# Kernel tuning notes

Measured on AMD Instinct MI355X. Metric: run time of the kernel, lower is better.

## Reference

```python
import jax, jax.numpy as jnp
import numpy as np

B, N, D_IN, D, H, L, NQ, NC, HID = 4, 25000, 32, 256, 8, 6, 100, 18, 1024


def _ln(x, g, b, eps=1e-5):
    m = jnp.mean(x, -1, keepdims=True)
    v = jnp.mean((x - m) ** 2, -1, keepdims=True)
    return (x - m) / jnp.sqrt(v + eps) * g + b


def _mha(q, kv, wqkv, bqkv, wo, bo, h):
    # q: (B, Lq, d), kv: (B, Lk, d); torch nn.MultiheadAttention math
    d = q.shape[-1]
    dh = d // h
    wq, wk, wv = jnp.split(wqkv, 3, axis=0)
    bq, bk, bv = jnp.split(bqkv, 3)
    Q = (q @ wq.T + bq).reshape(q.shape[0], q.shape[1], h, dh)
    K = (kv @ wk.T + bk).reshape(kv.shape[0], kv.shape[1], h, dh)
    V = (kv @ wv.T + bv).reshape(kv.shape[0], kv.shape[1], h, dh)
    s = jnp.einsum('bqhd,bkhd->bhqk', Q, K) / jnp.asarray(np.sqrt(dh), Q.dtype)
    a = jax.nn.softmax(s, axis=-1)
    o = jnp.einsum('bhqk,bkhd->bqhd', a, V).reshape(q.shape)
    return o @ wo.T + bo


def setup_inputs() -> dict:
    key = jax.random.key(0)
    ks = list(jax.random.split(key, 20))
    ki = iter(ks)

    def p(shape, s=0.02):
        return jax.random.normal(next(ki), shape, jnp.float32) * s

    inp = {
        'x': jax.random.normal(next(ki), (B * N, D_IN), jnp.float32),
        'batch_offsets': jnp.arange(B + 1, dtype=jnp.int32) * N,
        'ip_w': p((D, D_IN)), 'ip_b': jnp.zeros((D,), jnp.float32),
        'ip_ln_g': jnp.ones((D,), jnp.float32), 'ip_ln_b': jnp.zeros((D,), jnp.float32),
        'xm_w1': p((D, D_IN)), 'xm_b1': jnp.zeros((D,), jnp.float32),
        'xm_w2': p((D, D)), 'xm_b2': jnp.zeros((D,), jnp.float32),
        'query_embed': p((NQ, D), 1.0),
        'ca_wqkv': p((L, 3 * D, D)), 'ca_bqkv': jnp.zeros((L, 3 * D), jnp.float32),
        'ca_wo': p((L, D, D)), 'ca_bo': jnp.zeros((L, D), jnp.float32),
        'sa_wqkv': p((L, 3 * D, D)), 'sa_bqkv': jnp.zeros((L, 3 * D), jnp.float32),
        'sa_wo': p((L, D, D)), 'sa_bo': jnp.zeros((L, D), jnp.float32),
        'sa_ln_g': jnp.ones((L, D), jnp.float32), 'sa_ln_b': jnp.zeros((L, D), jnp.float32),
        'ffn_w1': p((L, HID, D)), 'ffn_b1': jnp.zeros((L, HID), jnp.float32),
        'ffn_w2': p((L, D, HID)), 'ffn_b2': jnp.zeros((L, D), jnp.float32),
        'ffn_ln_g': jnp.ones((L, D), jnp.float32), 'ffn_ln_b': jnp.zeros((L, D), jnp.float32),
        'out_ln_g': jnp.ones((D,), jnp.float32), 'out_ln_b': jnp.zeros((D,), jnp.float32),
        'cls_w1': p((D, D)), 'cls_b1': jnp.zeros((D,), jnp.float32),
        'cls_w2': p((NC + 1, D)), 'cls_b2': jnp.zeros((NC + 1,), jnp.float32),
    }
    return inp


def reference(x, batch_offsets, ip_w, ip_b, ip_ln_g, ip_ln_b, xm_w1, xm_b1, xm_w2, xm_b2,
              query_embed, ca_wqkv, ca_bqkv, ca_wo, ca_bo, sa_wqkv, sa_bqkv, sa_wo, sa_bo,
              sa_ln_g, sa_ln_b, ffn_w1, ffn_b1, ffn_w2, ffn_b2, ffn_ln_g, ffn_ln_b,
              out_ln_g, out_ln_b, cls_w1, cls_b1, cls_w2, cls_b2):
    b = batch_offsets.shape[0] - 1  # uniform segments -> batched attention
    n = x.shape[0] // b
    # input_proj: Linear -> LayerNorm -> ReLU
    inst = jax.nn.relu(_ln(x @ ip_w.T + ip_b, ip_ln_g, ip_ln_b)).reshape(b, n, -1)
    # x_mask: Linear -> ReLU -> Linear
    mask_feats = (jax.nn.relu(x @ xm_w1.T + xm_b1) @ xm_w2.T + xm_b2).reshape(b, n, -1)
    query = jnp.broadcast_to(query_embed, (b,) + query_embed.shape)
    for i in range(ca_wqkv.shape[0]):
        # CrossAttentionLayer: NOTE original discards dropout/norm results -> pure residual
        query = _mha(query, inst, ca_wqkv[i], ca_bqkv[i], ca_wo[i], ca_bo[i], H) + query
        # SelfAttentionLayer: residual + LayerNorm
        query = _ln(_mha(query, query, sa_wqkv[i], sa_bqkv[i], sa_wo[i], sa_bo[i], H) + query,
                    sa_ln_g[i], sa_ln_b[i])
        # FFN: residual + LayerNorm
        ff = jax.nn.relu(query @ ffn_w1[i].T + ffn_b1[i]) @ ffn_w2[i].T + ffn_b2[i]
        query = _ln(ff + query, ffn_ln_g[i], ffn_ln_b[i])
    qn = _ln(query, out_ln_g, out_ln_b)
    pred_labels = jax.nn.relu(qn @ cls_w1.T + cls_b1) @ cls_w2.T + cls_b2  # (b, NQ, NC+1)
    pred_masks = jnp.einsum('bqd,bnd->bqn', qn, mask_feats)  # (b, NQ, n)
    return pred_labels, pred_masks
```

## Files before the change

### kernel.cpp

```cpp
#include <hip/hip_runtime.h>

typedef unsigned short u16;
typedef unsigned int   u32;

constexpr int Bz   = 4;
constexpr int Ni   = 25000;
constexpr int BNi  = Bz * Ni;
constexpr int DIN  = 32;
constexpr int D    = 256;
constexpr int Hh   = 8;
constexpr int DH   = 32;
constexpr int Ll   = 6;
constexpr int NQ   = 100;
constexpr int NC1  = 19;
constexpr int HIDd = 1024;

constexpr int CHUNK  = 625;
constexpr int NCHUNK = Ni / CHUNK;
constexpr size_t PARTB = (size_t)Hh * NCHUNK * 128 * 34;
constexpr float SM_SCALE = 0.17677669529663687f;

__device__ __forceinline__ u16 f2b(float f) {
    union { float f; u32 u; } c; c.f = f;
    u32 u = c.u + 0x7FFFu + ((c.u >> 16) & 1u);
    return (u16)(u >> 16);
}

__global__ void k_cvt(const float* __restrict__ in, u16* __restrict__ out, int n) {
    for (int i = blockIdx.x * blockDim.x + threadIdx.x; i < n; i += gridDim.x * blockDim.x)
        out[i] = f2b(in[i]);
}

typedef __attribute__((ext_vector_type(8))) __bf16 bf8v;
typedef __attribute__((ext_vector_type(8))) short  s8v;
typedef __attribute__((ext_vector_type(4))) float  f4v;

template<bool DOLN>
__global__ __launch_bounds__(512) void k_inproj(
    const float* __restrict__ x, int row0, int Mloc,
    const u16* __restrict__ w16, const float* __restrict__ bias,
    const float* __restrict__ g, const float* __restrict__ bb,
    u16* __restrict__ outb)
{
    __shared__ u16 Ws[256 * 40];
    __shared__ float Cb[256], Cg[256], Cbb[256];
    const int tid = threadIdx.x, lane = tid & 63, w = tid >> 6;
    const int lr = lane & 15, hi = lane >> 4;

    for (int ch = tid; ch < 1024; ch += 512) {
        int r = ch >> 2, g4 = ch & 3;
        *(uint4*)&Ws[r * 40 + g4 * 8] = *(const uint4*)(w16 + r * 32 + g4 * 8);
    }
    if (tid < 256) {
        Cb[tid] = bias[tid];
        if (DOLN) { Cg[tid] = g[tid]; Cbb[tid] = bb[tid]; }
    }

    const int rloc = blockIdx.x * 128 + w * 16 + lr;
    const int gr = row0 + min(rloc, Mloc - 1);
    bf8v xf;
    {
        const float* xp = x + (size_t)gr * DIN + hi * 8;
        float4 a = *(const float4*)xp, c = *(const float4*)(xp + 4);
        union { s8v s; bf8v b; } u;
        u.s[0] = (short)f2b(a.x); u.s[1] = (short)f2b(a.y);
        u.s[2] = (short)f2b(a.z); u.s[3] = (short)f2b(a.w);
        u.s[4] = (short)f2b(c.x); u.s[5] = (short)f2b(c.y);
        u.s[6] = (short)f2b(c.z); u.s[7] = (short)f2b(c.w);
        xf = u.b;
    }
    __syncthreads();

    f4v acc[16];
    #pragma unroll
    for (int ci = 0; ci < 16; ci++) {
        acc[ci] = (f4v){0.f, 0.f, 0.f, 0.f};
        bf8v af = *(const bf8v*)&Ws[(ci * 16 + lr) * 40 + hi * 8];
        acc[ci] = __builtin_amdgcn_mfma_f32_16x16x32_bf16(af, xf, acc[ci], 0, 0, 0);
    }
    #pragma unroll
    for (int ci = 0; ci < 16; ci++)
        #pragma unroll
        for (int r = 0; r < 4; r++)
            acc[ci][r] += Cb[ci * 16 + hi * 4 + r];

    float mean = 0.f, ri = 1.f;
    if (DOLN) {
        float s = 0.f, q = 0.f;
        #pragma unroll
        for (int ci = 0; ci < 16; ci++)
            #pragma unroll
            for (int r = 0; r < 4; r++) { s += acc[ci][r]; q += acc[ci][r] * acc[ci][r]; }
        s += __shfl_xor(s, 16); s += __shfl_xor(s, 32);
        q += __shfl_xor(q, 16); q += __shfl_xor(q, 32);
        mean = s * (1.f / D);
        float var = q * (1.f / D) - mean * mean;
        ri = rsqrtf(var + 1e-5f);
    }
    if (rloc < Mloc) {
        #pragma unroll
        for (int ci = 0; ci < 16; ci++) {
            u16 o[4];
            #pragma unroll
            for (int r = 0; r < 4; r++) {
                float v = acc[ci][r];
                if (DOLN) v = (v - mean) * ri * Cg[ci * 16 + hi * 4 + r] + Cbb[ci * 16 + hi * 4 + r];
                o[r] = f2b(fmaxf(v, 0.f));
            }
            uint2 pk;
            pk.x = (u32)o[0] | ((u32)o[1] << 16);
            pk.y = (u32)o[2] | ((u32)o[3] << 16);
            *(uint2*)&outb[(size_t)rloc * 256 + ci * 16 + hi * 4] = pk;
        }
    }
}

__global__ __launch_bounds__(256) void k_ln(
    const float* __restrict__ in, float* __restrict__ out,
    const float* __restrict__ g, const float* __restrict__ b)
{
    const int t = threadIdx.x;
    const int row = blockIdx.x;
    float v = in[(size_t)row * D + t];
    float s = v, q = v * v;
    #pragma unroll
    for (int off = 32; off >= 1; off >>= 1) { s += __shfl_xor(s, off); q += __shfl_xor(q, off); }
    __shared__ float red[2][4];
    const int wid = t >> 6;
    if ((t & 63) == 0) { red[0][wid] = s; red[1][wid] = q; }
    __syncthreads();
    float S = red[0][0] + red[0][1] + red[0][2] + red[0][3];
    float Q = red[1][0] + red[1][1] + red[1][2] + red[1][3];
    float m   = S * (1.f / D);
    float var = Q * (1.f / D) - m * m;
    float ri  = rsqrtf(var + 1e-5f);
    out[(size_t)row * D + t] = (v - m) * ri * g[t] + b[t];
}

__global__ __launch_bounds__(256) void k_bcast(const float* __restrict__ qe, float* __restrict__ q)
{
    const int t = threadIdx.x;
    const int r = blockIdx.x;
    q[(size_t)r * D + t] = qe[(size_t)(r % NQ) * D + t];
}

template<int BM, int BN, int TM, int TN>
__global__ __launch_bounds__(256) void k_gemm(
    const float* __restrict__ A, const float* __restrict__ W,
    const float* __restrict__ bias, const float* __restrict__ resid,
    float* __restrict__ C, int M, int N, int K, int relu)
{
    constexpr int BK = 16;
    constexpr int TX = BN / TN, TY = BM / TM;
    static_assert(TX * TY == 256, "block must be 256 threads");
    __shared__ float As[BK][BM + 4];
    __shared__ float Ws[BK][BN + 4];

    const int tid = threadIdx.x;
    const int tx = tid % TX, ty = tid / TX;
    const int row0 = blockIdx.y * BM, col0 = blockIdx.x * BN;

    float acc[TM][TN];
    #pragma unroll
    for (int i = 0; i < TM; i++)
        #pragma unroll
        for (int j = 0; j < TN; j++) acc[i][j] = 0.f;

    for (int k0 = 0; k0 < K; k0 += BK) {
        __syncthreads();
        for (int idx = tid; idx < BM * (BK / 4); idx += 256) {
            int r = idx / (BK / 4), c4 = idx % (BK / 4);
            int gr = row0 + r;
            float4 v;
            if (gr < M) v = *(const float4*)(A + (size_t)gr * K + k0 + c4 * 4);
            else { v.x = v.y = v.z = v.w = 0.f; }
            As[c4*4+0][r] = v.x; As[c4*4+1][r] = v.y; As[c4*4+2][r] = v.z; As[c4*4+3][r] = v.w;
        }
        for (int idx = tid; idx < BN * (BK / 4); idx += 256) {
            int n = idx / (BK / 4), c4 = idx % (BK / 4);
            int gn = col0 + n;
            float4 v;
            if (gn < N) v = *(const float4*)(W + (size_t)gn * K + k0 + c4 * 4);
            else { v.x = v.y = v.z = v.w = 0.f; }
            Ws[c4*4+0][n] = v.x; Ws[c4*4+1][n] = v.y; Ws[c4*4+2][n] = v.z; Ws[c4*4+3][n] = v.w;
        }
        __syncthreads();
        #pragma unroll
        for (int kk = 0; kk < BK; kk++) {
            float a[TM], bb[TN];
            #pragma unroll
            for (int i = 0; i < TM; i++) a[i] = As[kk][ty * TM + i];
            #pragma unroll
            for (int j = 0; j < TN; j++) bb[j] = Ws[kk][tx * TN + j];
            #pragma unroll
            for (int i = 0; i < TM; i++)
                #pragma unroll
                for (int j = 0; j < TN; j++)
                    acc[i][j] = fmaf(a[i], bb[j], acc[i][j]);
        }
    }

    #pragma unroll
    for (int i = 0; i < TM; i++) {
        int gr = row0 + ty * TM + i;
        if (gr >= M) continue;
        #pragma unroll
        for (int j = 0; j < TN; j++) {
            int gn = col0 + tx * TN + j;
            if (gn >= N) continue;
            float v = acc[i][j];
            if (bias)  v += bias[gn];
            if (resid) v += resid[(size_t)gr * N + gn];
            if (relu)  v = fmaxf(v, 0.f);
            C[(size_t)gr * N + gn] = v;
        }
    }
}

template<bool RELU>
__global__ __launch_bounds__(256) void mm_small(
    const float* __restrict__ A, const u16* __restrict__ W,
    const float* __restrict__ bias, const float* __restrict__ resid,
    float* __restrict__ C, int M, int N, int K)
{
    __shared__ u16 As[64 * 40];
    __shared__ u16 Bs[64 * 40];
    const int tid  = threadIdx.x;
    const int lane = tid & 63, w = tid >> 6;
    const int wm = w >> 1, wn = w & 1;
    const int row0 = blockIdx.y * 64, col0 = blockIdx.x * 64;
    const int lr = lane & 15, hi = lane >> 4;

    f4v acc[2][2];
    #pragma unroll
    for (int i = 0; i < 2; i++)
        #pragma unroll
        for (int j = 0; j < 2; j++) acc[i][j] = (f4v){0.f, 0.f, 0.f, 0.f};

    const int sr = tid >> 2, sc = (tid & 3) * 8;
    const int ga = min(row0 + sr, M - 1);
    const int gw = min(col0 + sr, N - 1);

    for (int k0 = 0; k0 < K; k0 += 32) {
        __syncthreads();
        {
            const float* ap = A + (size_t)ga * K + k0 + sc;
            float4 a = *(const float4*)ap, c = *(const float4*)(ap + 4);
            union { s8v s; uint4 u; } cv;
            cv.s[0] = (short)f2b(a.x); cv.s[1] = (short)f2b(a.y);
            cv.s[2] = (short)f2b(a.z); cv.s[3] = (short)f2b(a.w);
            cv.s[4] = (short)f2b(c.x); cv.s[5] = (short)f2b(c.y);
            cv.s[6] = (short)f2b(c.z); cv.s[7] = (short)f2b(c.w);
            *(uint4*)&As[sr * 40 + sc] = cv.u;
            *(uint4*)&Bs[sr * 40 + sc] = *(const uint4*)(W + (size_t)gw * K + k0 + sc);
        }
        __syncthreads();
        bf8v a0 = *(const bf8v*)&As[(wm * 32      + lr) * 40 + hi * 8];
        bf8v a1 = *(const bf8v*)&As[(wm * 32 + 16 + lr) * 40 + hi * 8];
        bf8v b0 = *(const bf8v*)&Bs[(wn * 32      + lr) * 40 + hi * 8];
        bf8v b1 = *(const bf8v*)&Bs[(wn * 32 + 16 + lr) * 40 + hi * 8];
        acc[0][0] = __builtin_amdgcn_mfma_f32_16x16x32_bf16(a0, b0, acc[0][0], 0, 0, 0);
        acc[0][1] = __builtin_amdgcn_mfma_f32_16x16x32_bf16(a0, b1, acc[0][1], 0, 0, 0);
        acc[1][0] = __builtin_amdgcn_mfma_f32_16x16x32_bf16(a1, b0, acc[1][0], 0, 0, 0);
        acc[1][1] = __builtin_amdgcn_mfma_f32_16x16x32_bf16(a1, b1, acc[1][1], 0, 0, 0);
    }

    const int crl = hi * 4, ccl = lr;
    #pragma unroll
    for (int mi = 0; mi < 2; mi++)
        #pragma unroll
        for (int ni = 0; ni < 2; ni++)
            #pragma unroll
            for (int r = 0; r < 4; r++) {
                int grow = row0 + wm * 32 + mi * 16 + crl + r;
                int gcol = col0 + wn * 32 + ni * 16 + ccl;
                if (grow < M && gcol < N) {
                    float v = acc[mi][ni][r];
                    if (bias)  v += bias[gcol];
                    if (resid) v += resid[(size_t)grow * N + gcol];
                    if (RELU)  v = fmaxf(v, 0.f);
                    C[(size_t)grow * N + gcol] = v;
                }
            }
}

template<bool OUTBF>
__global__ __launch_bounds__(256) void mm128(
    const u16* __restrict__ A, const u16* __restrict__ W,
    const float* __restrict__ bias, void* __restrict__ Cv,
    int M, int N, int K, long long sA, long long sW, long long sC)
{
    __shared__ u16 As[128 * 40];
    __shared__ u16 Bs[128 * 40];
    A += (size_t)blockIdx.z * sA;
    W += (size_t)blockIdx.z * sW;
    const int tid = threadIdx.x, lane = tid & 63, w = tid >> 6;
    const int wm = w >> 1, wn = w & 1;
    const int row0 = blockIdx.y * 128, col0 = blockIdx.x * 128;
    const int lr = lane & 15, hi = lane >> 4;

    f4v acc[4][4];
    #pragma unroll
    for (int i = 0; i < 4; i++)
        #pragma unroll
        for (int j = 0; j < 4; j++) acc[i][j] = (f4v){0.f, 0.f, 0.f, 0.f};

    for (int k0 = 0; k0 < K; k0 += 32) {
        __syncthreads();
        #pragma unroll
        for (int i = 0; i < 2; i++) {
            int idx = tid + i * 256;
            int r = idx >> 2, kc = idx & 3;
            int ga = min(row0 + r, M - 1);
            int gb = min(col0 + r, N - 1);
            *(uint4*)&As[r * 40 + kc * 8] = *(const uint4*)(A + (size_t)ga * K + k0 + kc * 8);
            *(uint4*)&Bs[r * 40 + kc * 8] = *(const uint4*)(W + (size_t)gb * K + k0 + kc * 8);
        }
        __syncthreads();
        bf8v a[4], bb[4];
        #pragma unroll
        for (int mi = 0; mi < 4; mi++)
            a[mi] = *(const bf8v*)&As[(wm * 64 + mi * 16 + lr) * 40 + hi * 8];
        #pragma unroll
        for (int ni = 0; ni < 4; ni++)
            bb[ni] = *(const bf8v*)&Bs[(wn * 64 + ni * 16 + lr) * 40 + hi * 8];
        #pragma unroll
        for (int mi = 0; mi < 4; mi++)
            #pragma unroll
            for (int ni = 0; ni < 4; ni++)
                acc[mi][ni] = __builtin_amdgcn_mfma_f32_16x16x32_bf16(a[mi], bb[ni], acc[mi][ni], 0, 0, 0);
    }

    const int crl = hi * 4, ccl = lr;
    #pragma unroll
    for (int mi = 0; mi < 4; mi++)
        #pragma unroll
        for (int ni = 0; ni < 4; ni++)
            #pragma unroll
            for (int r = 0; r < 4; r++) {
                int grow = row0 + wm * 64 + mi * 16 + crl + r;
                int gcol = col0 + wn * 64 + ni * 16 + ccl;
                if (grow < M && gcol < N) {
                    float v = acc[mi][ni][r];
                    if (bias) v += bias[gcol];
                    if (OUTBF) ((u16*)Cv)[(size_t)blockIdx.z * sC + (size_t)grow * N + gcol] = f2b(v);
                    else       ((float*)Cv)[(size_t)blockIdx.z * sC + (size_t)grow * N + gcol] = v;
                }
            }
}

__global__ __launch_bounds__(512) void k_flash(
    const float* __restrict__ qbuf, const u16* __restrict__ kv,
    float* __restrict__ part, int bBase, size_t kvStride, size_t pStride)
{
    const int tid = threadIdx.x;
    const int lane = tid & 63, w = tid >> 6;
    const int h = blockIdx.y;
    const int b = bBase + blockIdx.z;
    const u16* kvp = kv + (size_t)blockIdx.z * kvStride;
    float* pp = part + (size_t)blockIdx.z * pStride;
    const int k0loc = blockIdx.x * CHUNK;
    const int lr = lane & 15, hi = lane >> 4;

    __shared__ u16 Ks[64 * 40];
    __shared__ u16 Vt[32 * 72];
    __shared__ u16 Pt[8][16 * 72];

    const int qt = w * 16 + lr;
    const int qg = b * NQ + min(qt, NQ - 1);
    bf8v qf;
    {
        const float* Qp = qbuf + (size_t)qg * D + h * DH + hi * 8;
        union { s8v s; bf8v b; } qu;
        #pragma unroll
        for (int j = 0; j < 8; j++) qu.s[j] = (short)f2b(Qp[j] * SM_SCALE);
        qf = qu.b;
    }

    float m = -1e30f, l = 0.f;
    f4v o0 = (f4v){0.f,0.f,0.f,0.f}, o1 = (f4v){0.f,0.f,0.f,0.f};

    constexpr int NSTEP = (CHUNK + 63) / 64;
    for (int s = 0; s < NSTEP; s++) {
        const int ck = k0loc + s * 64;
        const int nv = min(64, k0loc + CHUNK - ck);
        __syncthreads();
        if (tid < 256) {
            int key = tid >> 2, g = tid & 3;
            int krow = min(ck + key, Ni - 1);
            *(uint4*)&Ks[key * 40 + g * 8] =
                *(const uint4*)(kvp + (size_t)krow * (2 * D) + h * DH + g * 8);
        } else {
            int t2 = tid - 256;
            int key = t2 >> 2, g = t2 & 3;
            int krow = min(ck + key, Ni - 1);
            uint4 u = *(const uint4*)(kvp + (size_t)krow * (2 * D) + D + h * DH + g * 8);
            const u16* pu = (const u16*)&u;
            #pragma unroll
            for (int j = 0; j < 8; j++) Vt[(g * 8 + j) * 72 + key] = pu[j];
        }
        __syncthreads();

        f4v sf[4];
        #pragma unroll
        for (int j = 0; j < 4; j++) {
            bf8v kf = *(const bf8v*)&Ks[(j * 16 + lr) * 40 + hi * 8];
            sf[j] = (f4v){0.f,0.f,0.f,0.f};
            sf[j] = __builtin_amdgcn_mfma_f32_16x16x32_bf16(kf, qf, sf[j], 0, 0, 0);
        }

        float sv[16];
        #pragma unroll
        for (int j = 0; j < 4; j++)
            #pragma unroll
            for (int r = 0; r < 4; r++) {
                int key0 = j * 16 + hi * 4 + r;
                sv[j * 4 + r] = (key0 < nv) ? sf[j][r] : -1e30f;
            }
        float smax = sv[0];
        #pragma unroll
        for (int j = 1; j < 16; j++) smax = fmaxf(smax, sv[j]);
        smax = fmaxf(smax, __shfl_xor(smax, 16));
        smax = fmaxf(smax, __shfl_xor(smax, 32));
        float mnew  = fmaxf(m, smax);
        float scale = __expf(m - mnew);
        m = mnew;

        float psum = 0.f;
        u16 pb[16];
        #pragma unroll
        for (int j = 0; j < 16; j++) {
            float p = __expf(sv[j] - mnew);
            psum += p;
            pb[j] = f2b(p);
        }
        psum += __shfl_xor(psum, 16);
        psum += __shfl_xor(psum, 32);
        l = l * scale + psum;

        u16* pw = &Pt[w][lr * 72];
        #pragma unroll
        for (int j = 0; j < 4; j++) {
            *(u32*)&pw[j * 16 + hi * 4]     = (u32)pb[j*4+0] | ((u32)pb[j*4+1] << 16);
            *(u32*)&pw[j * 16 + hi * 4 + 2] = (u32)pb[j*4+2] | ((u32)pb[j*4+3] << 16);
        }

        const int qb4 = hi * 4;
        float f0 = __shfl(scale, qb4 + 0);
        float f1 = __shfl(scale, qb4 + 1);
        float f2 = __shfl(scale, qb4 + 2);
        float f3 = __shfl(scale, qb4 + 3);
        o0[0] *= f0; o0[1] *= f1; o0[2] *= f2; o0[3] *= f3;
        o1[0] *= f0; o1[1] *= f1; o1[2] *= f2; o1[3] *= f3;

        #pragma unroll
        for (int j = 0; j < 2; j++) {
            bf8v pf  = *(const bf8v*)&Pt[w][lr * 72 + j * 32 + hi * 8];
            bf8v vf0 = *(const bf8v*)&Vt[lr * 72 + j * 32 + hi * 8];
            bf8v vf1 = *(const bf8v*)&Vt[(16 + lr) * 72 + j * 32 + hi * 8];
            o0 = __builtin_amdgcn_mfma_f32_16x16x32_bf16(pf, vf0, o0, 0, 0, 0);
            o1 = __builtin_amdgcn_mfma_f32_16x16x32_bf16(pf, vf1, o1, 0, 0, 0);
        }
    }

    const size_t pbase = ((size_t)(h * NCHUNK + blockIdx.x) * 128) * 34;
    #pragma unroll
    for (int r = 0; r < 4; r++) {
        int qtr = w * 16 + hi * 4 + r;
        pp[pbase + (size_t)qtr * 34 + 2 + lr]      = o0[r];
        pp[pbase + (size_t)qtr * 34 + 2 + 16 + lr] = o1[r];
    }
    if (lane < 16) {
        pp[pbase + (size_t)(w * 16 + lane) * 34 + 0] = m;
        pp[pbase + (size_t)(w * 16 + lane) * 34 + 1] = l;
    }
}

__global__ __launch_bounds__(64) void k_fmerge(const float* __restrict__ part,
                                               float* __restrict__ abuf, int bBase, size_t pStride)
{
    const float* pz = part + (size_t)blockIdx.y * pStride;
    const int b = bBase + blockIdx.y;
    const int t = threadIdx.x;
    const int hq = blockIdx.x;
    const int h = hq / NQ, q = hq % NQ;
    float mmax = -1e30f;
    for (int c = 0; c < NCHUNK; c++)
        mmax = fmaxf(mmax, pz[((size_t)(h * NCHUNK + c) * 128 + q) * 34]);
    float L = 0.f, a = 0.f;
    for (int c = 0; c < NCHUNK; c++) {
        const float* p = &pz[((size_t)(h * NCHUNK + c) * 128 + q) * 34];
        float wv = __expf(p[0] - mmax);
        L += wv * p[1];
        if (t < DH) a += wv * p[2 + t];
    }
    if (t < DH)
        abuf[((size_t)(b * NQ + q)) * D + h * DH + t] = a / L;
}

__global__ __launch_bounds__(128) void k_sattn(const float* __restrict__ sqkv, float* __restrict__ abuf)
{
    const int tid = threadIdx.x;
    const int bh = blockIdx.x;
    const int b = bh >> 3, h = bh & 7;
    __shared__ float Ks[NQ][DH], Vs[NQ][DH];
    for (int idx = tid; idx < NQ * 8; idx += 128) {
        int kk = idx >> 3, f4 = idx & 7;
        const float* base = sqkv + ((size_t)(b * NQ + kk)) * (3 * D) + h * DH;
        *(float4*)&Ks[kk][f4 * 4] = *(const float4*)(base + D + f4 * 4);
        *(float4*)&Vs[kk][f4 * 4] = *(const float4*)(base + 2 * D + f4 * 4);
    }
    float qr[DH];
    const int q = tid;
    if (q < NQ) {
        const float* Qp = sqkv + ((size_t)(b * NQ + q)) * (3 * D) + h * DH;
        #pragma unroll
        for (int d = 0; d < DH; d += 4) {
            float4 v = *(const float4*)(Qp + d);
            qr[d] = v.x * SM_SCALE; qr[d+1] = v.y * SM_SCALE;
            qr[d+2] = v.z * SM_SCALE; qr[d+3] = v.w * SM_SCALE;
        }
    } else {
        #pragma unroll
        for (int d = 0; d < DH; d++) qr[d] = 0.f;
    }
    __syncthreads();
    float m = -1e30f, l = 0.f, acc[DH];
    #pragma unroll
    for (int d = 0; d < DH; d++) acc[d] = 0.f;
    for (int kk = 0; kk < NQ; kk++) {
        float sc = 0.f;
        #pragma unroll
        for (int d = 0; d < DH; d++) sc += qr[d] * Ks[kk][d];
        if (sc > m) {
            float r = __expf(m - sc);
            l *= r;
            #pragma unroll
            for (int d = 0; d < DH; d++) acc[d] *= r;
            m = sc;
        }
        float p = __expf(sc - m);
        l += p;
        #pragma unroll
        for (int d = 0; d < DH; d++) acc[d] += p * Vs[kk][d];
    }
    if (q < NQ) {
        float li = 1.f / l;
        float* o = abuf + ((size_t)(b * NQ + q)) * D + h * DH;
        #pragma unroll
        for (int d = 0; d < DH; d++) o[d] = acc[d] * li;
    }
}

extern "C" void kernel_launch(void* const* d_in, const int* in_sizes, int n_in,
                              void* d_out, int out_size, void* d_ws, size_t ws_size,
                              hipStream_t stream)
{
    const float* x        = (const float*)d_in[0];
    const float* ip_w     = (const float*)d_in[2];
    const float* ip_b     = (const float*)d_in[3];
    const float* ip_g     = (const float*)d_in[4];
    const float* ip_bb    = (const float*)d_in[5];
    const float* xm_w1    = (const float*)d_in[6];
    const float* xm_b1    = (const float*)d_in[7];
    const float* xm_w2    = (const float*)d_in[8];
    const float* xm_b2    = (const float*)d_in[9];
    const float* qe       = (const float*)d_in[10];
    const float* ca_wqkv  = (const float*)d_in[11];
    const float* ca_bqkv  = (const float*)d_in[12];
    const float* ca_wo    = (const float*)d_in[13];
    const float* ca_bo    = (const float*)d_in[14];
    const float* sa_wqkv  = (const float*)d_in[15];
    const float* sa_bqkv  = (const float*)d_in[16];
    const float* sa_wo    = (const float*)d_in[17];
    const float* sa_bo    = (const float*)d_in[18];
    const float* sa_ln_g  = (const float*)d_in[19];
    const float* sa_ln_b  = (const float*)d_in[20];
    const float* ffn_w1   = (const float*)d_in[21];
    const float* ffn_b1   = (const float*)d_in[22];
    const float* ffn_w2   = (const float*)d_in[23];
    const float* ffn_b2   = (const float*)d_in[24];
    const float* ffn_ln_g = (const float*)d_in[25];
    const float* ffn_ln_b = (const float*)d_in[26];
    const float* out_ln_g = (const float*)d_in[27];
    const float* out_ln_b = (const float*)d_in[28];
    const float* cls_w1   = (const float*)d_in[29];
    const float* cls_b1   = (const float*)d_in[30];
    const float* cls_w2   = (const float*)d_in[31];
    const float* cls_b2   = (const float*)d_in[32];
    float* out = (float*)d_out;

    bool batched = false;
    int instRows;
    if      (ws_size >= 210000000ull) { batched = true; instRows = BNi; }
    else if (ws_size >= 112000000ull) { instRows = BNi; }
    else if (ws_size >=  73000000ull) { instRows = Ni;  }
    else return;
    const bool instFull = (instRows == BNi);
    const int nzb = batched ? Bz : 1;

    char* wp = (char*)d_ws;
    auto alloc = [&](size_t bytes) -> char* {
        char* r = wp; wp += (bytes + 255) & ~(size_t)255; return r;
    };
    u16*   instb = (u16*)  alloc((size_t)instRows * D * 2);
    u16*   kvb   = (u16*)  alloc((size_t)(batched ? BNi : Ni) * 2 * D * 2);
    float* part  = (float*)alloc((size_t)nzb * PARTB * 4);
    float* qbuf  = (float*)alloc(409600);
    float* abuf  = (float*)alloc(409600);
    float* sqkv  = (float*)alloc(1228800);
    float* f1b   = (float*)alloc(1638400);
    float* qA    = (float*)alloc(409600);
    float* qB    = (float*)alloc(409600);
    u16*   ipw16 = (u16*)  alloc(256 * 32 * 2);
    u16*   xw116 = (u16*)  alloc(256 * 32 * 2);
    u16*   xw216 = (u16*)  alloc((size_t)D * D * 2);
    u16*   caq16 = (u16*)  alloc((size_t)Ll * 3 * D * D * 2);
    u16*   saq16 = (u16*)  alloc((size_t)Ll * 3 * D * D * 2);
    u16*   cao16 = (u16*)  alloc((size_t)Ll * D * D * 2);
    u16*   sao16 = (u16*)  alloc((size_t)Ll * D * D * 2);
    u16*   fw116 = (u16*)  alloc((size_t)Ll * HIDd * D * 2);
    u16*   fw216 = (u16*)  alloc((size_t)Ll * D * HIDd * 2);
    u16*   qnb   = (u16*)  alloc((size_t)Bz * NQ * D * 2);

    k_cvt<<<16,   256, 0, stream>>>(ip_w,  ipw16, 256 * 32);
    k_cvt<<<16,   256, 0, stream>>>(xm_w1, xw116, 256 * 32);
    k_cvt<<<64,   256, 0, stream>>>(xm_w2, xw216, D * D);
    k_cvt<<<1024, 256, 0, stream>>>(ca_wqkv, caq16, Ll * 3 * D * D);
    k_cvt<<<1024, 256, 0, stream>>>(sa_wqkv, saq16, Ll * 3 * D * D);
    k_cvt<<<512,  256, 0, stream>>>(ca_wo, cao16, Ll * D * D);
    k_cvt<<<512,  256, 0, stream>>>(sa_wo, sao16, Ll * D * D);
    k_cvt<<<1024, 256, 0, stream>>>(ffn_w1, fw116, Ll * HIDd * D);
    k_cvt<<<1024, 256, 0, stream>>>(ffn_w2, fw216, Ll * D * HIDd);

    if (instFull)
        k_inproj<true><<<(BNi + 127) / 128, 512, 0, stream>>>(
            x, 0, BNi, ipw16, ip_b, ip_g, ip_bb, instb);
    k_bcast<<<Bz * NQ, 256, 0, stream>>>(qe, qA);

    float* qcur = qA;
    float* qtmp = qB;
    for (int i = 0; i < Ll; i++) {
        const u16*   wq16 = caq16 + (size_t)i * 3 * D * D;
        const u16*   wkv16 = wq16 + (size_t)D * D;
        const float* bqkv = ca_bqkv + (size_t)i * 3 * D;
        mm_small<false><<<dim3(4, 7), 256, 0, stream>>>(
            qcur, wq16, bqkv, nullptr, qbuf, Bz * NQ, D, D);
        if (batched) {
            mm128<true><<<dim3(4, 196, 4), 256, 0, stream>>>(
                instb, wkv16, bqkv + D, kvb, Ni, 2 * D, D,
                (long long)Ni * D, 0, (long long)Ni * 2 * D);
            k_flash<<<dim3(NCHUNK, Hh, 4), 512, 0, stream>>>(
                qbuf, kvb, part, 0, (size_t)Ni * 2 * D, PARTB);
            k_fmerge<<<dim3(Hh * NQ, 4), 64, 0, stream>>>(part, abuf, 0, PARTB);
        } else {
            for (int b = 0; b < Bz; b++) {
                if (!instFull)
                    k_inproj<true><<<(Ni + 127) / 128, 512, 0, stream>>>(
                        x, b * Ni, Ni, ipw16, ip_b, ip_g, ip_bb, instb);
                const u16* ip = instFull ? instb + (size_t)b * Ni * D : instb;
                mm128<true><<<dim3(4, 196, 1), 256, 0, stream>>>(
                    ip, wkv16, bqkv + D, kvb, Ni, 2 * D, D, 0, 0, 0);
                k_flash<<<dim3(NCHUNK, Hh, 1), 512, 0, stream>>>(
                    qbuf, kvb, part, b, 0, 0);
                k_fmerge<<<dim3(Hh * NQ, 1), 64, 0, stream>>>(part, abuf, b, 0);
            }
        }
        mm_small<false><<<dim3(4, 7), 256, 0, stream>>>(
            abuf, cao16 + (size_t)i * D * D, ca_bo + (size_t)i * D, qcur, qtmp,
            Bz * NQ, D, D);
        { float* t2 = qcur; qcur = qtmp; qtmp = t2; }
        mm_small<false><<<dim3(12, 7), 256, 0, stream>>>(
            qcur, saq16 + (size_t)i * 3 * D * D, sa_bqkv + (size_t)i * 3 * D, nullptr, sqkv,
            Bz * NQ, 3 * D, D);
        k_sattn<<<Bz * Hh, 128, 0, stream>>>(sqkv, abuf);
        mm_small<false><<<dim3(4, 7), 256, 0, stream>>>(
            abuf, sao16 + (size_t)i * D * D, sa_bo + (size_t)i * D, qcur, qtmp,
            Bz * NQ, D, D);
        k_ln<<<Bz * NQ, 256, 0, stream>>>(qtmp, qtmp, sa_ln_g + i * D, sa_ln_b + i * D);
        { float* t2 = qcur; qcur = qtmp; qtmp = t2; }
        mm_small<true><<<dim3(16, 7), 256, 0, stream>>>(
            qcur, fw116 + (size_t)i * HIDd * D, ffn_b1 + (size_t)i * HIDd, nullptr, f1b,
            Bz * NQ, HIDd, D);
        mm_small<false><<<dim3(4, 7), 256, 0, stream>>>(
            f1b, fw216 + (size_t)i * D * HIDd, ffn_b2 + (size_t)i * D, qcur, qtmp,
            Bz * NQ, D, HIDd);
        k_ln<<<Bz * NQ, 256, 0, stream>>>(qtmp, qtmp, ffn_ln_g + i * D, ffn_ln_b + i * D);
        { float* t2 = qcur; qcur = qtmp; qtmp = t2; }
    }

    float* qn = qbuf;
    k_ln<<<Bz * NQ, 256, 0, stream>>>(qcur, qn, out_ln_g, out_ln_b);
    k_gemm<64,64,4,4><<<dim3(4, 7), 256, 0, stream>>>(
        qn, cls_w1, cls_b1, nullptr, abuf, Bz * NQ, D, D, 1);
    k_gemm<64,64,4,4><<<dim3(1, 7), 256, 0, stream>>>(
        abuf, cls_w2, cls_b2, nullptr, out, Bz * NQ, NC1, D, 0);

    k_cvt<<<128, 256, 0, stream>>>(qn, qnb, Bz * NQ * D);
    if (instFull) {
        k_inproj<false><<<(BNi + 127) / 128, 512, 0, stream>>>(
            x, 0, BNi, xw116, xm_b1, nullptr, nullptr, instb);
        if (batched) {
            mm128<true><<<dim3(2, 196, 4), 256, 0, stream>>>(
                instb, xw216, xm_b2, kvb, Ni, D, D,
                (long long)Ni * D, 0, (long long)Ni * D);
            mm128<false><<<dim3(196, 1, 4), 256, 0, stream>>>(
                qnb, kvb, nullptr, out + Bz * NQ * NC1, NQ, Ni, D,
                (long long)NQ * D, (long long)Ni * D, (long long)NQ * Ni);
        } else {
            for (int b = 0; b < Bz; b++) {
                mm128<true><<<dim3(2, 196, 1), 256, 0, stream>>>(
                    instb + (size_t)b * Ni * D, xw216, xm_b2, kvb, Ni, D, D, 0, 0, 0);
                mm128<false><<<dim3(196, 1, 1), 256, 0, stream>>>(
                    qnb + (size_t)b * NQ * D, kvb, nullptr,
                    out + Bz * NQ * NC1 + (size_t)b * NQ * Ni, NQ, Ni, D, 0, 0, 0);
            }
        }
    } else {
        for (int b = 0; b < Bz; b++) {
            k_inproj<false><<<(Ni + 127) / 128, 512, 0, stream>>>(
                x, b * Ni, Ni, xw116, xm_b1, nullptr, nullptr, instb);
            mm128<true><<<dim3(2, 196, 1), 256, 0, stream>>>(
                instb, xw216, xm_b2, kvb, Ni, D, D, 0, 0, 0);
            mm128<false><<<dim3(196, 1, 1), 256, 0, stream>>>(
                qnb + (size_t)b * NQ * D, kvb, nullptr,
                out + Bz * NQ * NC1 + (size_t)b * NQ * Ni, NQ, Ni, D, 0, 0, 0);
        }
    }
}
```

Before: 1.992 ms.

## Fuse small GEMMs with LayerNorm and use direct-to-LDS loads with XCD swizzle in mm128

Adds an mm_tail kernel that computes a full 256-column row block per workgroup, so bias, residual and LayerNorm are applied in the epilogue. This replaces the separate mm_small plus k_ln launches in the decoder loop and removes extra launches and round trips through global memory. mm128 now stages tiles through global_load_lds into unpadded LDS and remaps block indices so neighbouring tiles land on the same XCD. The trade-offs are fewer workgroups (7) for the small GEMMs, possible LDS bank conflicts from dropping the padding, and a one-pass variance formula that is less numerically stable.

```diff
diff --git a/kernel.cpp b/kernel.cpp
--- a/kernel.cpp
+++ b/kernel.cpp
@@ -29,6 +29,12 @@
 __global__ void k_cvt(const float* __restrict__ in, u16* __restrict__ out, int n) {
     for (int i = blockIdx.x * blockDim.x + threadIdx.x; i < n; i += gridDim.x * blockDim.x)
         out[i] = f2b(in[i]);
+}
+
+__device__ __forceinline__ void gload16(const u16* g, u16* l) {
+    __builtin_amdgcn_global_load_lds(
+        (const __attribute__((address_space(1))) void*)g,
+        (__attribute__((address_space(3))) void*)l, 16, 0, 0);
 }
 
 typedef __attribute__((ext_vector_type(8))) __bf16 bf8v;
@@ -284,21 +290,163 @@
             }
 }
 
+template<bool DOLN>
+__global__ __launch_bounds__(256) void mm_tail(
+    const float* __restrict__ A, const u16* __restrict__ W,
+    const float* __restrict__ bias, const float* __restrict__ resid,
+    const float* __restrict__ g, const float* __restrict__ bb,
+    float* __restrict__ C, int M, int K)
+{
+    __shared__ u16 As[64 * 40];
+    __shared__ u16 Bs[256 * 40];
+    __shared__ float sred[4][64], qred[4][64];
+    const int tid = threadIdx.x, lane = tid & 63, w = tid >> 6;
+    const int row0 = blockIdx.x * 64;
+    const int lr = lane & 15, hi = lane >> 4;
+
+    f4v acc[4][4];
+    #pragma unroll
+    for (int i = 0; i < 4; i++)
+        #pragma unroll
+        for (int j = 0; j < 4; j++) acc[i][j] = (f4v){0.f, 0.f, 0.f, 0.f};
+
+    const int sr = tid >> 2, sc = (tid & 3) * 8;
+    const int ga = min(row0 + sr, M - 1);
+
+    for (int k0 = 0; k0 < K; k0 += 32) {
+        __syncthreads();
+        {
+            const float* ap = A + (size_t)ga * K + k0 + sc;
+            float4 a = *(const float4*)ap, c = *(const float4*)(ap + 4);
+            union { s8v s; uint4 u; } cv;
+            cv.s[0] = (short)f2b(a.x); cv.s[1] = (short)f2b(a.y);
+            cv.s[2] = (short)f2b(a.z); cv.s[3] = (short)f2b(a.w);
+            cv.s[4] = (short)f2b(c.x); cv.s[5] = (short)f2b(c.y);
+            cv.s[6] = (short)f2b(c.z); cv.s[7] = (short)f2b(c.w);
+            *(uint4*)&As[sr * 40 + sc] = cv.u;
+            const u16* wrow = W + (size_t)tid * K + k0;
+            #pragma unroll
+            for (int c4 = 0; c4 < 4; c4++)
+                *(uint4*)&Bs[tid * 40 + c4 * 8] = *(const uint4*)(wrow + c4 * 8);
+        }
+        __syncthreads();
+        bf8v a[4], b[4];
+        #pragma unroll
+        for (int mi = 0; mi < 4; mi++)
+            a[mi] = *(const bf8v*)&As[(mi * 16 + lr) * 40 + hi * 8];
+        #pragma unroll
+        for (int ni = 0; ni < 4; ni++)
+            b[ni] = *(const bf8v*)&Bs[(w * 64 + ni * 16 + lr) * 40 + hi * 8];
+        #pragma unroll
+        for (int mi = 0; mi < 4; mi++)
+            #pragma unroll
+            for (int ni = 0; ni < 4; ni++)
+                acc[mi][ni] = __builtin_amdgcn_mfma_f32_16x16x32_bf16(a[mi], b[ni], acc[mi][ni], 0, 0, 0);
+    }
+
+    float v[4][4][4];
+    #pragma unroll
+    for (int mi = 0; mi < 4; mi++)
+        #pragma unroll
+        for (int ni = 0; ni < 4; ni++) {
+            int gcol = w * 64 + ni * 16 + lr;
+            #pragma unroll
+            for (int r = 0; r < 4; r++) {
+                int grow = min(row0 + mi * 16 + hi * 4 + r, M - 1);
+                float vv = acc[mi][ni][r];
+                if (bias)  vv += bias[gcol];
+                if (resid) vv += resid[(size_t)grow * 256 + gcol];
+                v[mi][ni][r] = vv;
+            }
+        }
+
+    float mean[4][4], rinv[4][4];
+    if (DOLN) {
+        float rs[16], rq[16];
+        #pragma unroll
+        for (int mi = 0; mi < 4; mi++)
+            #pragma unroll
+            for (int r = 0; r < 4; r++) {
+                float s = 0.f, q = 0.f;
+                #pragma unroll
+                for (int ni = 0; ni < 4; ni++) { s += v[mi][ni][r]; q += v[mi][ni][r] * v[mi][ni][r]; }
+                rs[mi * 4 + r] = s; rq[mi * 4 + r] = q;
+            }
+        #pragma unroll
+        for (int off = 1; off < 16; off <<= 1)
+            #pragma unroll
+            for (int i = 0; i < 16; i++) {
+                rs[i] += __shfl_xor(rs[i], off);
+                rq[i] += __shfl_xor(rq[i], off);
+            }
+        if (lr == 0) {
+            #pragma unroll
+            for (int mi = 0; mi < 4; mi++)
+                #pragma unroll
+                for (int r = 0; r < 4; r++) {
+                    sred[w][mi * 16 + hi * 4 + r] = rs[mi * 4 + r];
+                    qred[w][mi * 16 + hi * 4 + r] = rq[mi * 4 + r];
+                }
+        }
+        __syncthreads();
+        #pragma unroll
+        for (int mi = 0; mi < 4; mi++)
+            #pragma unroll
+            for (int r = 0; r < 4; r++) {
+                int row = mi * 16 + hi * 4 + r;
+                float S = sred[0][row] + sred[1][row] + sred[2][row] + sred[3][row];
+                float Q = qred[0][row] + qred[1][row] + qred[2][row] + qred[3][row];
+                float m  = S * (1.f / 256.f);
+                float va = Q * (1.f / 256.f) - m * m;
+                mean[mi][r] = m;
+                rinv[mi][r] = rsqrtf(va + 1e-5f);
+            }
+    }
+
+    #pragma unroll
+    for (int mi = 0; mi < 4; mi++)
+        #pragma unroll
+        for (int ni = 0; ni < 4; ni++) {
+            int gcol = w * 64 + ni * 16 + lr;
+            float gg = DOLN ? g[gcol] : 0.f, bbv = DOLN ? bb[gcol] : 0.f;
+            #pragma unroll
+            for (int r = 0; r < 4; r++) {
+                int grow = row0 + mi * 16 + hi * 4 + r;
+                if (grow < M) {
+                    float vv = v[mi][ni][r];
+                    if (DOLN) vv = (vv - mean[mi][r]) * rinv[mi][r] * gg + bbv;
+                    C[(size_t)grow * 256 + gcol] = vv;
+                }
+            }
+        }
+}
+
 template<bool OUTBF>
 __global__ __launch_bounds__(256) void mm128(
     const u16* __restrict__ A, const u16* __restrict__ W,
     const float* __restrict__ bias, void* __restrict__ Cv,
     int M, int N, int K, long long sA, long long sW, long long sC)
 {
-    __shared__ u16 As[128 * 40];
-    __shared__ u16 Bs[128 * 40];
-    A += (size_t)blockIdx.z * sA;
-    W += (size_t)blockIdx.z * sW;
+    __shared__ u16 As[128 * 32];
+    __shared__ u16 Bs[128 * 32];
+
+    const int gx = gridDim.x, gy = gridDim.y;
+    const int total = gx * gy * (int)gridDim.z;
+    const int flat = blockIdx.x + gx * (blockIdx.y + gy * blockIdx.z);
+    const int q8 = total >> 3, r8 = total & 7;
+    const int xcd = flat & 7, blk = flat >> 3;
+    const int swz = (xcd < r8 ? xcd * (q8 + 1) : r8 * (q8 + 1) + (xcd - r8) * q8) + blk;
+    const int bx = swz % gx, by = (swz / gx) % gy, bz = swz / (gx * gy);
+
+    A += (size_t)bz * sA;
+    W += (size_t)bz * sW;
     const int tid = threadIdx.x, lane = tid & 63, w = tid >> 6;
     const int wm = w >> 1, wn = w & 1;
-    const int row0 = blockIdx.y * 128, col0 = blockIdx.x * 128;
+    const int row0 = by * 128, col0 = bx * 128;
     const int lr = lane & 15, hi = lane >> 4;
 
+    const int srow = lane >> 2, scol = (lane & 3) * 8;
+
     f4v acc[4][4];
     #pragma unroll
     for (int i = 0; i < 4; i++)
@@ -309,21 +457,21 @@
         __syncthreads();
         #pragma unroll
         for (int i = 0; i < 2; i++) {
-            int idx = tid + i * 256;
-            int r = idx >> 2, kc = idx & 3;
-            int ga = min(row0 + r, M - 1);
-            int gb = min(col0 + r, N - 1);
-            *(uint4*)&As[r * 40 + kc * 8] = *(const uint4*)(A + (size_t)ga * K + k0 + kc * 8);
-            *(uint4*)&Bs[r * 40 + kc * 8] = *(const uint4*)(W + (size_t)gb * K + k0 + kc * 8);
+            const int c = w * 2 + i;
+            const int row = c * 16 + srow;
+            const int gra = min(row0 + row, M - 1);
+            const int grb = min(col0 + row, N - 1);
+            gload16(A + (size_t)gra * K + k0 + scol, &As[c * 512]);
+            gload16(W + (size_t)grb * K + k0 + scol, &Bs[c * 512]);
         }
         __syncthreads();
         bf8v a[4], bb[4];
         #pragma unroll
         for (int mi = 0; mi < 4; mi++)
-            a[mi] = *(const bf8v*)&As[(wm * 64 + mi * 16 + lr) * 40 + hi * 8];
+            a[mi] = *(const bf8v*)&As[(wm * 64 + mi * 16 + lr) * 32 + hi * 8];
         #pragma unroll
         for (int ni = 0; ni < 4; ni++)
-            bb[ni] = *(const bf8v*)&Bs[(wn * 64 + ni * 16 + lr) * 40 + hi * 8];
+            bb[ni] = *(const bf8v*)&Bs[(wn * 64 + ni * 16 + lr) * 32 + hi * 8];
         #pragma unroll
         for (int mi = 0; mi < 4; mi++)
             #pragma unroll
@@ -343,8 +491,8 @@
                 if (grow < M && gcol < N) {
                     float v = acc[mi][ni][r];
                     if (bias) v += bias[gcol];
-                    if (OUTBF) ((u16*)Cv)[(size_t)blockIdx.z * sC + (size_t)grow * N + gcol] = f2b(v);
-                    else       ((float*)Cv)[(size_t)blockIdx.z * sC + (size_t)grow * N + gcol] = v;
+                    if (OUTBF) ((u16*)Cv)[(size_t)bz * sC + (size_t)grow * N + gcol] = f2b(v);
+                    else       ((float*)Cv)[(size_t)bz * sC + (size_t)grow * N + gcol] = v;
                 }
             }
 }
@@ -641,11 +789,11 @@
     float* qcur = qA;
     float* qtmp = qB;
     for (int i = 0; i < Ll; i++) {
-        const u16*   wq16 = caq16 + (size_t)i * 3 * D * D;
+        const u16*   wq16  = caq16 + (size_t)i * 3 * D * D;
         const u16*   wkv16 = wq16 + (size_t)D * D;
-        const float* bqkv = ca_bqkv + (size_t)i * 3 * D;
-        mm_small<false><<<dim3(4, 7), 256, 0, stream>>>(
-            qcur, wq16, bqkv, nullptr, qbuf, Bz * NQ, D, D);
+        const float* bqkv  = ca_bqkv + (size_t)i * 3 * D;
+        mm_tail<false><<<7, 256, 0, stream>>>(
+            qcur, wq16, bqkv, nullptr, nullptr, nullptr, qbuf, Bz * NQ, D);
         if (batched) {
             mm128<true><<<dim3(4, 196, 4), 256, 0, stream>>>(
                 instb, wkv16, bqkv + D, kvb, Ni, 2 * D, D,
@@ -666,26 +814,24 @@
                 k_fmerge<<<dim3(Hh * NQ, 1), 64, 0, stream>>>(part, abuf, b, 0);
             }
         }
-        mm_small<false><<<dim3(4, 7), 256, 0, stream>>>(
-            abuf, cao16 + (size_t)i * D * D, ca_bo + (size_t)i * D, qcur, qtmp,
-            Bz * NQ, D, D);
+        mm_tail<false><<<7, 256, 0, stream>>>(
+            abuf, cao16 + (size_t)i * D * D, ca_bo + (size_t)i * D, qcur,
+            nullptr, nullptr, qtmp, Bz * NQ, D);
         { float* t2 = qcur; qcur = qtmp; qtmp = t2; }
         mm_small<false><<<dim3(12, 7), 256, 0, stream>>>(
             qcur, saq16 + (size_t)i * 3 * D * D, sa_bqkv + (size_t)i * 3 * D, nullptr, sqkv,
             Bz * NQ, 3 * D, D);
         k_sattn<<<Bz * Hh, 128, 0, stream>>>(sqkv, abuf);
-        mm_small<false><<<dim3(4, 7), 256, 0, stream>>>(
-            abuf, sao16 + (size_t)i * D * D, sa_bo + (size_t)i * D, qcur, qtmp,
-            Bz * NQ, D, D);
-        k_ln<<<Bz * NQ, 256, 0, stream>>>(qtmp, qtmp, sa_ln_g + i * D, sa_ln_b + i * D);
+        mm_tail<true><<<7, 256, 0, stream>>>(
+            abuf, sao16 + (size_t)i * D * D, sa_bo + (size_t)i * D, qcur,
+            sa_ln_g + i * D, sa_ln_b + i * D, qtmp, Bz * NQ, D);
         { float* t2 = qcur; qcur = qtmp; qtmp = t2; }
         mm_small<true><<<dim3(16, 7), 256, 0, stream>>>(
             qcur, fw116 + (size_t)i * HIDd * D, ffn_b1 + (size_t)i * HIDd, nullptr, f1b,
             Bz * NQ, HIDd, D);
-        mm_small<false><<<dim3(4, 7), 256, 0, stream>>>(
-            f1b, fw216 + (size_t)i * D * HIDd, ffn_b2 + (size_t)i * D, qcur, qtmp,
-            Bz * NQ, D, HIDd);
-        k_ln<<<Bz * NQ, 256, 0, stream>>>(qtmp, qtmp, ffn_ln_g + i * D, ffn_ln_b + i * D);
+        mm_tail<true><<<7, 256, 0, stream>>>(
+            f1b, fw216 + (size_t)i * D * HIDd, ffn_b2 + (size_t)i * D, qcur,
+            ffn_ln_g + i * D, ffn_ln_b + i * D, qtmp, Bz * NQ, HIDd);
         { float* t2 = qcur; qcur = qtmp; qtmp = t2; }
     }
 
```

After: 2.386 ms. +19.8%, slower.
